# Performance work log

Measured on AMD Instinct MI355X. Metric: run time of the kernel, lower is better.

The kernel has to match this reference:

```python
import jax, jax.numpy as jnp
import numpy as np

LN_EPS = 1e-5
NUM_HEADS = 16

def _layernorm(x, g, b):
    mu = jnp.mean(x, axis=-1, keepdims=True)
    var = jnp.mean(jnp.square(x - mu), axis=-1, keepdims=True)
    return (x - mu) * jax.lax.rsqrt(var + LN_EPS) * g + b

def setup_inputs() -> dict:
    key = jax.random.key(0)
    ks = jax.random.split(key, 8)
    B, N, C, Hf = 8, 4096, 1024, 2048
    s = 1.0 / np.sqrt(C)
    return {
        "x": jax.random.normal(ks[0], (B, N, C), jnp.float32),
        "ln1_g": jnp.ones((C,), jnp.float32),
        "ln1_b": jnp.zeros((C,), jnp.float32),
        "ln2_g": jnp.ones((C,), jnp.float32),
        "ln2_b": jnp.zeros((C,), jnp.float32),
        "wq": jax.random.normal(ks[1], (C, C), jnp.float32) * s,
        "wk": jax.random.normal(ks[2], (C, C), jnp.float32) * s,
        "wv": jax.random.normal(ks[3], (C, C), jnp.float32) * s,
        "proj_w": jax.random.normal(ks[4], (C, C), jnp.float32) * s,
        "proj_b": jnp.zeros((C,), jnp.float32),
        "fc1_w": jax.random.normal(ks[5], (C, Hf), jnp.float32) * s,
        "fc1_b": jnp.zeros((Hf,), jnp.float32),
        "fc2_w": jax.random.normal(ks[6], (Hf, C), jnp.float32) / np.sqrt(Hf),
        "fc2_b": jnp.zeros((C,), jnp.float32),
    }

def reference(x, ln1_g, ln1_b, ln2_g, ln2_b, wq, wk, wv, proj_w, proj_b,
              fc1_w, fc1_b, fc2_w, fc2_b):
    B, N, C = x.shape
    H = NUM_HEADS
    d = C // H
    scale = d ** -0.5

    # --- attention branch (note: attention over the head_dim axis, d x d scores) ---
    h = _layernorm(x, ln1_g, ln1_b)
    def split(t):  # (B,N,C) -> (B,H,d,N), matching permute(0,2,3,1)
        return jnp.transpose(t.reshape(B, N, H, d), (0, 2, 3, 1))
    q = split(h @ wq)
    k = split(h @ wk)
    v = split(h @ wv)
    attn = jax.nn.softmax(jnp.einsum("bhdn,bhen->bhde", q, k) * scale, axis=-1)  # (B,H,d,d)
    o = jnp.einsum("bhde,bhen->bhdn", attn, v)           # (B,H,d,N)
    o = jnp.transpose(o, (0, 2, 1, 3)).reshape(B, N, C)  # transpose(1,2).reshape
    x = x + (o @ proj_w + proj_b)

    # --- MLP branch ---
    h2 = _layernorm(x, ln2_g, ln2_b)
    h2 = jax.nn.gelu(h2 @ fc1_w + fc1_b, approximate=False)
    x = x + (h2 @ fc2_w + fc2_b)
    return x
```

## Files before the change

### kernel.cpp

```cpp
#include <hip/hip_runtime.h>
#include <cmath>

typedef __attribute__((ext_vector_type(8))) _Float16 f16x8;
typedef __attribute__((ext_vector_type(8))) unsigned short u16x8;
typedef __attribute__((ext_vector_type(4))) float f32x4;

__device__ __forceinline__ unsigned short f2h(float f) {
  return __builtin_bit_cast(unsigned short, (_Float16)f);
}
__device__ __forceinline__ float h2f(unsigned short u) {
  return (float)__builtin_bit_cast(_Float16, u);
}

__device__ __forceinline__ void async16(const void* gp, void* lp) {
  __builtin_amdgcn_global_load_lds(
      (const __attribute__((address_space(1))) void*)gp,
      (__attribute__((address_space(3))) void*)lp, 16, 0, 0);
}

__global__ __launch_bounds__(256) void transpose_cast(
    const float* __restrict__ W, unsigned short* __restrict__ WT, int K, int N) {
  __shared__ float tile[32][33];
  const int tx = threadIdx.x & 31, ty = threadIdx.x >> 5;
  const int n0 = blockIdx.x * 32, k0 = blockIdx.y * 32;
#pragma unroll
  for (int r = 0; r < 4; ++r)
    tile[ty + 8 * r][tx] = W[(size_t)(k0 + ty + 8 * r) * N + n0 + tx];
  __syncthreads();
#pragma unroll
  for (int r = 0; r < 4; ++r)
    WT[(size_t)(n0 + ty + 8 * r) * K + k0 + tx] = f2h(tile[tx][ty + 8 * r]);
}

__global__ __launch_bounds__(256) void layernorm_cast(
    const float* __restrict__ x, const float* __restrict__ g,
    const float* __restrict__ bt, unsigned short* __restrict__ out) {
  const int row = blockIdx.x, tid = threadIdx.x;
  const float4 v = ((const float4*)(x + (size_t)row * 1024))[tid];
  float s = v.x + v.y + v.z + v.w;
  float ss = v.x * v.x + v.y * v.y + v.z * v.z + v.w * v.w;
#pragma unroll
  for (int off = 32; off >= 1; off >>= 1) {
    s += __shfl_down(s, off);
    ss += __shfl_down(ss, off);
  }
  __shared__ float red[10];
  const int wave = tid >> 6, lane = tid & 63;
  if (lane == 0) { red[wave] = s; red[4 + wave] = ss; }
  __syncthreads();
  if (tid == 0) {
    float S = red[0] + red[1] + red[2] + red[3];
    float SS = red[4] + red[5] + red[6] + red[7];
    float mu = S * (1.f / 1024.f);
    float var = SS * (1.f / 1024.f) - mu * mu;
    red[8] = mu;
    red[9] = rsqrtf(var + 1e-5f);
  }
  __syncthreads();
  const float mu = red[8], rs = red[9];
  const float4 gv = ((const float4*)g)[tid];
  const float4 bv = ((const float4*)bt)[tid];
  ushort4 r;
  r.x = f2h((v.x - mu) * rs * gv.x + bv.x);
  r.y = f2h((v.y - mu) * rs * gv.y + bv.y);
  r.z = f2h((v.z - mu) * rs * gv.z + bv.z);
  r.w = f2h((v.w - mu) * rs * gv.w + bv.w);
  ((ushort4*)(out + (size_t)row * 1024))[tid] = r;
}

__global__ __launch_bounds__(256) void resid_ln(
    const float* __restrict__ x, const unsigned short* __restrict__ pr,
    const float* __restrict__ pb, const float* __restrict__ g,
    const float* __restrict__ bt, float* __restrict__ out,
    unsigned short* __restrict__ h2) {
  const int row = blockIdx.x, tid = threadIdx.x;
  const size_t off = (size_t)row * 1024;
  const float4 xv = ((const float4*)(x + off))[tid];
  const ushort4 pv = ((const ushort4*)(pr + off))[tid];
  const float4 bb = ((const float4*)pb)[tid];
  float4 v;
  v.x = xv.x + h2f(pv.x) + bb.x;
  v.y = xv.y + h2f(pv.y) + bb.y;
  v.z = xv.z + h2f(pv.z) + bb.z;
  v.w = xv.w + h2f(pv.w) + bb.w;
  ((float4*)(out + off))[tid] = v;
  float s = v.x + v.y + v.z + v.w;
  float ss = v.x * v.x + v.y * v.y + v.z * v.z + v.w * v.w;
#pragma unroll
  for (int o = 32; o >= 1; o >>= 1) {
    s += __shfl_down(s, o);
    ss += __shfl_down(ss, o);
  }
  __shared__ float red[10];
  const int wave = tid >> 6, lane = tid & 63;
  if (lane == 0) { red[wave] = s; red[4 + wave] = ss; }
  __syncthreads();
  if (tid == 0) {
    float S = red[0] + red[1] + red[2] + red[3];
    float SS = red[4] + red[5] + red[6] + red[7];
    float mu = S * (1.f / 1024.f);
    float var = SS * (1.f / 1024.f) - mu * mu;
    red[8] = mu;
    red[9] = rsqrtf(var + 1e-5f);
  }
  __syncthreads();
  const float mu = red[8], rs = red[9];
  const float4 gv = ((const float4*)g)[tid];
  const float4 bv = ((const float4*)bt)[tid];
  ushort4 r;
  r.x = f2h((v.x - mu) * rs * gv.x + bv.x);
  r.y = f2h((v.y - mu) * rs * gv.y + bv.y);
  r.z = f2h((v.z - mu) * rs * gv.z + bv.z);
  r.w = f2h((v.w - mu) * rs * gv.w + bv.w);
  ((ushort4*)(h2 + off))[tid] = r;
}

__global__ __launch_bounds__(256) void resid_add(
    float* __restrict__ out, const unsigned short* __restrict__ y,
    const float* __restrict__ b) {
  const int row = blockIdx.x, tid = threadIdx.x;
  const size_t off = (size_t)row * 1024;
  float4 o = ((const float4*)(out + off))[tid];
  const ushort4 yv = ((const ushort4*)(y + off))[tid];
  const float4 bv = ((const float4*)b)[tid];
  o.x += h2f(yv.x) + bv.x;
  o.y += h2f(yv.y) + bv.y;
  o.z += h2f(yv.z) + bv.z;
  o.w += h2f(yv.w) + bv.w;
  ((float4*)(out + off))[tid] = o;
}

__global__ __launch_bounds__(256) void gemm_bt(
    const unsigned short* __restrict__ A, const unsigned short* __restrict__ BT,
    int M, int N, int K,
    const float* __restrict__ bias, unsigned short* __restrict__ outB, int gelu) {
  __shared__ unsigned short smem[17408];
  unsigned short* sA = smem;
  unsigned short* sB = smem + 8192;
  const int tid = threadIdx.x, wave = tid >> 6, lane = tid & 63;
  const int l16 = lane & 15, g16 = lane >> 4;
  const int wm = wave & 1, wn = wave >> 1;

  const int lin = blockIdx.y * gridDim.x + blockIdx.x;
  const int t_ = lin >> 3;
  const int bx = t_ % gridDim.x;
  const int by = (lin & 7) + 8 * (t_ / gridDim.x);
  const int row0 = by * 128, col0 = bx * 128;

  const int r_ = tid >> 2;
  const int s_ = ((tid & 3) ^ ((tid >> 3) & 3)) * 8;
  const unsigned short* pA = A + (size_t)(row0 + r_) * K + s_;
  const unsigned short* pB = BT + (size_t)(col0 + r_) * K + s_;
  unsigned short* dA = sA + wave * 512;
  unsigned short* dB = sB + wave * 512;
  const size_t rstep = (size_t)64 * K;

  f32x4 acc[4][4] = {};

  for (int k0 = 0; k0 < K; k0 += 64) {
    __syncthreads();
    async16(pA, dA);
    async16(pA + rstep, dA + 2048);
    async16(pA + 32, dA + 4096);
    async16(pA + rstep + 32, dA + 6144);
    async16(pB, dB);
    async16(pB + rstep, dB + 2048);
    async16(pB + 32, dB + 4096);
    async16(pB + rstep + 32, dB + 6144);
    pA += 64;
    pB += 64;
    __syncthreads();
#pragma unroll
    for (int kk = 0; kk < 2; ++kk) {
      f16x8 af[4], bf[4];
#pragma unroll
      for (int i = 0; i < 4; ++i) {
        const int ra = wm * 64 + i * 16 + l16;
        af[i] = __builtin_bit_cast(f16x8,
            *(const u16x8*)&sA[kk * 4096 + ra * 32 + (g16 ^ ((ra >> 1) & 3)) * 8]);
      }
#pragma unroll
      for (int j = 0; j < 4; ++j) {
        const int rb = wn * 64 + j * 16 + l16;
        bf[j] = __builtin_bit_cast(f16x8,
            *(const u16x8*)&sB[kk * 4096 + rb * 32 + (g16 ^ ((rb >> 1) & 3)) * 8]);
      }
#pragma unroll
      for (int i = 0; i < 4; ++i)
#pragma unroll
        for (int j = 0; j < 4; ++j)
          acc[i][j] = __builtin_amdgcn_mfma_f32_16x16x32_f16(af[i], bf[j], acc[i][j], 0, 0, 0);
    }
  }

  __syncthreads();
  unsigned short* scr = smem + wave * 4352;
#pragma unroll
  for (int j = 0; j < 4; ++j) {
    const float bcol = gelu ? bias[col0 + wn * 64 + j * 16 + l16] : 0.f;
#pragma unroll
    for (int i = 0; i < 4; ++i)
#pragma unroll
      for (int r = 0; r < 4; ++r) {
        float val = acc[i][j][r] + bcol;
        if (gelu) val = 0.5f * val * (1.0f + erff(val * 0.70710678118f));
        scr[(i * 16 + g16 * 4 + r) * 68 + j * 16 + l16] = f2h(val);
      }
  }
#pragma unroll
  for (int rr = 0; rr < 8; ++rr) {
    const int lr = rr * 8 + (lane >> 3);
    const int lc = (lane & 7) * 8;
    const u16x8 val = *(const u16x8*)&scr[lr * 68 + lc];
    *(u16x8*)(outB + (size_t)(row0 + wm * 64 + lr) * N + col0 + wn * 64 + lc) = val;
  }
}


#define STAGE_A(TT, KKH)                                                       \
  {                                                                            \
    unsigned short* d = smem + ((TT) & 1) * 32768 + (KKH) * 8192 + wave * 512; \
    const unsigned short* sp_ = pA + (size_t)(TT) * 64 + (KKH) * 32;           \
    async16(sp_, d);                                                           \
    async16(sp_ + rstep, d + 4096);                                            \
  }

#define STAGE_B(TT, KKH)                                                       \
  {                                                                            \
    unsigned short* d =                                                        \
        smem + ((TT) & 1) * 32768 + 16384 + (KKH) * 8192 + wave * 512;         \
    const unsigned short* sp_ = pB + (size_t)(TT) * 64 + (KKH) * 32;           \
    async16(sp_, d);                                                           \
    async16(sp_ + rstep, d + 4096);                                            \
  }

#define GPHASE(KK, MH, STAGE, TAILW)                                           \
  {                                                                            \
    f16x8 af[4];                                                               \
    _Pragma("unroll") for (int i = 0; i < 4; ++i) {                            \
      const int ra = wm * 128 + ((MH)*4 + i) * 16 + l16;                       \
      af[i] = __builtin_bit_cast(                                              \
          f16x8, *(const u16x8*)&bufA[(KK)*8192 + ra * 32 +                    \
                                      ((g16 ^ ((ra >> 1) & 3)) * 8)]);         \
    }                                                                          \
    if ((MH) == 0) {                                                           \
      _Pragma("unroll") for (int j = 0; j < 4; ++j) {                          \
        const int rb = wn * 64 + j * 16 + l16;                                 \
        bf[j] = __builtin_bit_cast(                                            \
            f16x8, *(const u16x8*)&bufB[(KK)*8192 + rb * 32 +                  \
                                        ((g16 ^ ((rb >> 1) & 3)) * 8)]);       \
      }                                                                        \
    }                                                                          \
    STAGE;                                                                     \
    __builtin_amdgcn_s_barrier();                                              \
    asm volatile("s_waitcnt lgkmcnt(0)" ::: "memory");                         \
    __builtin_amdgcn_s_setprio(1);                                             \
    _Pragma("unroll") for (int i = 0; i < 4; ++i)                              \
        _Pragma("unroll") for (int j = 0; j < 4; ++j) acc[(MH)*4 + i][j] =     \
        __builtin_amdgcn_mfma_f32_16x16x32_f16(af[i], bf[j],                   \
                                               acc[(MH)*4 + i][j], 0, 0, 0);   \
    __builtin_amdgcn_s_setprio(0);                                             \
    TAILW;                                                                     \
    __builtin_amdgcn_s_barrier();                                              \
  }

__global__ __launch_bounds__(512) void gemm256(
    const unsigned short* __restrict__ A, const unsigned short* __restrict__ BT,
    int M, int N, int K,
    const float* __restrict__ bias, unsigned short* __restrict__ outB, int gelu) {
  __shared__ __align__(16) unsigned short smem[65536];
  const int tid = threadIdx.x, wave = tid >> 6, lane = tid & 63;
  const int l16 = lane & 15, g16 = lane >> 4;
  const int wm = wave >> 2, wn = wave & 3;

  const int lin = blockIdx.y * gridDim.x + blockIdx.x;
  const int t_ = lin >> 3;
  const int bx = t_ % gridDim.x;
  const int by = (lin & 7) + 8 * (t_ / gridDim.x);
  const int row0 = by * 256, col0 = bx * 256;

  const int r_ = tid >> 2;
  const int s_ = ((tid & 3) ^ ((tid >> 3) & 3)) * 8;
  const unsigned short* pA = A + (size_t)(row0 + r_) * K + s_;
  const unsigned short* pB = BT + (size_t)(col0 + r_) * K + s_;
  const size_t rstep = (size_t)128 * K;
  const int NT = K >> 6;

  f32x4 acc[8][4] = {};

  STAGE_B(0, 0);
  STAGE_A(0, 0);
  STAGE_B(0, 1);
  STAGE_A(0, 1);
  STAGE_B(1, 0);
  STAGE_A(1, 0);
  STAGE_B(1, 1);
  asm volatile("s_waitcnt vmcnt(6)" ::: "memory");
  __builtin_amdgcn_s_barrier();

  for (int t = 0; t < NT - 2; ++t) {
    const unsigned short* bufA = smem + (t & 1) * 32768;
    const unsigned short* bufB = bufA + 16384;
    f16x8 bf[4];
    GPHASE(0, 0, STAGE_A(t + 1, 1), )
    GPHASE(0, 1, STAGE_B(t + 2, 0), )
    GPHASE(1, 0, STAGE_A(t + 2, 0), )
    GPHASE(1, 1, STAGE_B(t + 2, 1),
           asm volatile("s_waitcnt vmcnt(6)" ::: "memory"))
  }

  {
    const int t = NT - 2;
    const unsigned short* bufA = smem + (t & 1) * 32768;
    const unsigned short* bufB = bufA + 16384;
    f16x8 bf[4];
    GPHASE(0, 0, STAGE_A(t + 1, 1), )
    GPHASE(0, 1, , )
    GPHASE(1, 0, , )
    GPHASE(1, 1, , asm volatile("s_waitcnt vmcnt(0)" ::: "memory"))
  }
  {
    const int t = NT - 1;
    const unsigned short* bufA = smem + (t & 1) * 32768;
    const unsigned short* bufB = bufA + 16384;
    f16x8 bf[4];
    GPHASE(0, 0, , )
    GPHASE(0, 1, , )
    GPHASE(1, 0, , )
    GPHASE(1, 1, , )
  }

  unsigned short* scr = smem + wave * 4352;
#pragma unroll
  for (int mh = 0; mh < 2; ++mh) {
#pragma unroll
    for (int j = 0; j < 4; ++j) {
      const float bcol = gelu ? bias[col0 + wn * 64 + j * 16 + l16] : 0.f;
#pragma unroll
      for (int i = 0; i < 4; ++i)
#pragma unroll
        for (int r = 0; r < 4; ++r) {
          float val = acc[mh * 4 + i][j][r] + bcol;
          if (gelu) val = 0.5f * val * (1.0f + erff(val * 0.70710678118f));
          scr[(i * 16 + g16 * 4 + r) * 68 + j * 16 + l16] = f2h(val);
        }
    }
#pragma unroll
    for (int rr = 0; rr < 8; ++rr) {
      const int lr = rr * 8 + (lane >> 3);
      const int lc = (lane & 7) * 8;
      const u16x8 val = *(const u16x8*)&scr[lr * 68 + lc];
      *(u16x8*)(outB + (size_t)(row0 + wm * 128 + mh * 64 + lr) * N + col0 +
                wn * 64 + lc) = val;
    }
  }
}

__global__ __launch_bounds__(256) void attn_qk_part(
    const unsigned short* __restrict__ qkv, float* __restrict__ sp) {
  constexpr int ST = 72;
  __shared__ unsigned short sQT[64 * ST];
  __shared__ unsigned short sKT[64 * ST];
  const int bx = blockIdx.x, bh = bx >> 2, chunk = bx & 3;
  const int b = bh >> 4, h = bh & 15;
  const size_t base = (size_t)b * 4096 * 3072 + (size_t)h * 64;
  const int tid = threadIdx.x, wave = tid >> 6, lane = tid & 63;
  const int l16 = lane & 15, g16 = lane >> 4;
  const int wm = wave & 1, wn = wave >> 1;
  const int srow = tid >> 2, sseg = tid & 3;

  f32x4 acc[2][2] = {};

  for (int ntl = 0; ntl < 16; ++ntl) {
    const int nt = chunk * 16 + ntl;
    __syncthreads();
    const size_t roff = base + (size_t)(nt * 64 + srow) * 3072 + sseg * 16;
    const u16x8 q0 = *(const u16x8*)(qkv + roff);
    const u16x8 q1 = *(const u16x8*)(qkv + roff + 8);
    const u16x8 k0 = *(const u16x8*)(qkv + roff + 1024);
    const u16x8 k1 = *(const u16x8*)(qkv + roff + 1032);
#pragma unroll
    for (int ii = 0; ii < 8; ++ii) {
      sQT[(sseg * 16 + ii) * ST + srow] = q0[ii];
      sQT[(sseg * 16 + 8 + ii) * ST + srow] = q1[ii];
      sKT[(sseg * 16 + ii) * ST + srow] = k0[ii];
      sKT[(sseg * 16 + 8 + ii) * ST + srow] = k1[ii];
    }
    __syncthreads();
#pragma unroll
    for (int kk = 0; kk < 2; ++kk) {
      f16x8 aq[2], bk[2];
#pragma unroll
      for (int i = 0; i < 2; ++i)
        aq[i] = __builtin_bit_cast(f16x8,
            *(const u16x8*)&sQT[(wm * 32 + i * 16 + l16) * ST + kk * 32 + g16 * 8]);
#pragma unroll
      for (int j = 0; j < 2; ++j)
        bk[j] = __builtin_bit_cast(f16x8,
            *(const u16x8*)&sKT[(wn * 32 + j * 16 + l16) * ST + kk * 32 + g16 * 8]);
#pragma unroll
      for (int i = 0; i < 2; ++i)
#pragma unroll
        for (int j = 0; j < 2; ++j)
          acc[i][j] = __builtin_amdgcn_mfma_f32_16x16x32_f16(aq[i], bk[j], acc[i][j], 0, 0, 0);
    }
  }

  float* o = sp + (size_t)bx * 4096;
#pragma unroll
  for (int i = 0; i < 2; ++i)
#pragma unroll
    for (int j = 0; j < 2; ++j)
#pragma unroll
      for (int r = 0; r < 4; ++r)
        o[(wm * 32 + i * 16 + g16 * 4 + r) * 64 + (wn * 32 + j * 16 + l16)] = acc[i][j][r];
}

__global__ __launch_bounds__(64) void attn_softmax(
    const float* __restrict__ sp, unsigned short* __restrict__ am) {
  const int bh = blockIdx.x, dd = threadIdx.x;
  const float* p = sp + (size_t)bh * 4 * 4096 + dd * 64;
  float row[64];
#pragma unroll
  for (int e4 = 0; e4 < 16; ++e4) {
    const float4 a = ((const float4*)p)[e4];
    const float4 b_ = ((const float4*)(p + 4096))[e4];
    const float4 c_ = ((const float4*)(p + 8192))[e4];
    const float4 d_ = ((const float4*)(p + 12288))[e4];
    row[4 * e4 + 0] = a.x + b_.x + c_.x + d_.x;
    row[4 * e4 + 1] = a.y + b_.y + c_.y + d_.y;
    row[4 * e4 + 2] = a.z + b_.z + c_.z + d_.z;
    row[4 * e4 + 3] = a.w + b_.w + c_.w + d_.w;
  }
  float mx = -1e30f;
#pragma unroll
  for (int e = 0; e < 64; ++e) mx = fmaxf(mx, row[e]);
  float sum = 0.f;
#pragma unroll
  for (int e = 0; e < 64; ++e) {
    row[e] = __expf(0.125f * (row[e] - mx));
    sum += row[e];
  }
  const float inv = 1.0f / sum;
  unsigned short* q = am + (size_t)bh * 4096 + dd * 64;
#pragma unroll
  for (int e = 0; e < 64; ++e) q[e] = f2h(row[e] * inv);
}

__global__ __launch_bounds__(256) void attn_pv(
    const unsigned short* __restrict__ qkv, const unsigned short* __restrict__ am,
    unsigned short* __restrict__ o) {
  const int bx = blockIdx.x, bh = bx >> 2, chunk = bx & 3;
  const int b = bh >> 4, h = bh & 15;
  const size_t base = (size_t)b * 4096 * 3072 + (size_t)h * 64;
  const int tid = threadIdx.x, wave = tid >> 6, lane = tid & 63;
  const int l16 = lane & 15, g16 = lane >> 4;
  const int wm = wave & 1, wn = wave >> 1;

  f16x8 amf[2][2];
#pragma unroll
  for (int i = 0; i < 2; ++i)
#pragma unroll
    for (int kk = 0; kk < 2; ++kk)
      amf[i][kk] = __builtin_bit_cast(f16x8,
          *(const u16x8*)(am + (size_t)bh * 4096 +
                          (wm * 32 + i * 16 + l16) * 64 + kk * 32 + g16 * 8));

  for (int ntl = 0; ntl < 16; ++ntl) {
    const int nt = chunk * 16 + ntl;
    f32x4 oc[2][2] = {};
#pragma unroll
    for (int kk = 0; kk < 2; ++kk) {
#pragma unroll
      for (int j = 0; j < 2; ++j) {
        const f16x8 vf = __builtin_bit_cast(f16x8,
            *(const u16x8*)(qkv + base + 2048 +
                            (size_t)(nt * 64 + wn * 32 + j * 16 + l16) * 3072 +
                            kk * 32 + g16 * 8));
#pragma unroll
        for (int i = 0; i < 2; ++i)
          oc[i][j] = __builtin_amdgcn_mfma_f32_16x16x32_f16(amf[i][kk], vf, oc[i][j], 0, 0, 0);
      }
    }
#pragma unroll
    for (int i = 0; i < 2; ++i)
#pragma unroll
      for (int j = 0; j < 2; ++j)
#pragma unroll
        for (int r = 0; r < 4; ++r) {
          const int dd = wm * 32 + i * 16 + g16 * 4 + r;
          const int nf = nt * 64 + wn * 32 + j * 16 + l16;
          const int row = b * 4096 + dd * 64 + h * 4 + (nf >> 10);
          o[(size_t)row * 1024 + (nf & 1023)] = f2h(oc[i][j][r]);
        }
  }
}

extern "C" void kernel_launch(void* const* d_in, const int* in_sizes, int n_in,
                              void* d_out, int out_size, void* d_ws, size_t ws_size,
                              hipStream_t stream) {
  (void)in_sizes; (void)n_in; (void)out_size; (void)ws_size;
  const float* x = (const float*)d_in[0];
  const float* ln1g = (const float*)d_in[1];
  const float* ln1b = (const float*)d_in[2];
  const float* ln2g = (const float*)d_in[3];
  const float* ln2b = (const float*)d_in[4];
  const float* wq = (const float*)d_in[5];
  const float* wk = (const float*)d_in[6];
  const float* wv = (const float*)d_in[7];
  const float* projw = (const float*)d_in[8];
  const float* projb = (const float*)d_in[9];
  const float* fc1w = (const float*)d_in[10];
  const float* fc1b = (const float*)d_in[11];
  const float* fc2w = (const float*)d_in[12];
  const float* fc2b = (const float*)d_in[13];
  float* out = (float*)d_out;

  const int M = 8 * 4096, C = 1024, HF = 2048;
  const size_t MC = (size_t)M * C;

  unsigned short* p = (unsigned short*)d_ws;
  unsigned short* wqkvT = p; p += (size_t)3 * C * C;
  unsigned short* prT = p; p += (size_t)C * C;
  unsigned short* f1T = p; p += (size_t)HF * C;
  unsigned short* f2T = p; p += (size_t)C * HF;
  unsigned short* hb = p;  p += MC;
  unsigned short* qkvb = p; p += 3 * MC;
  float* Spart = (float*)hb;
  unsigned short* Am = wqkvT;
  unsigned short* ob = hb;
  unsigned short* projout = qkvb;
  unsigned short* h2 = qkvb + 2 * MC;
  unsigned short* h3 = qkvb;
  unsigned short* yb = hb;

  transpose_cast<<<dim3(C / 32, C / 32), 256, 0, stream>>>(wq, wqkvT, C, C);
  transpose_cast<<<dim3(C / 32, C / 32), 256, 0, stream>>>(wk, wqkvT + (size_t)C * C, C, C);
  transpose_cast<<<dim3(C / 32, C / 32), 256, 0, stream>>>(wv, wqkvT + (size_t)2 * C * C, C, C);
  transpose_cast<<<dim3(C / 32, C / 32), 256, 0, stream>>>(projw, prT, C, C);
  transpose_cast<<<dim3(HF / 32, C / 32), 256, 0, stream>>>(fc1w, f1T, C, HF);
  transpose_cast<<<dim3(C / 32, HF / 32), 256, 0, stream>>>(fc2w, f2T, HF, C);

  layernorm_cast<<<M, 256, 0, stream>>>(x, ln1g, ln1b, hb);

  gemm256<<<dim3(3 * C / 256, M / 256), 512, 0, stream>>>(
      hb, wqkvT, M, 3 * C, C, nullptr, qkvb, 0);

  attn_qk_part<<<512, 256, 0, stream>>>(qkvb, Spart);
  attn_softmax<<<128, 64, 0, stream>>>(Spart, Am);
  attn_pv<<<512, 256, 0, stream>>>(qkvb, Am, ob);

  gemm_bt<<<dim3(C / 128, M / 128), 256, 0, stream>>>(
      ob, prT, M, C, C, nullptr, projout, 0);

  resid_ln<<<M, 256, 0, stream>>>(x, projout, projb, ln2g, ln2b, out, h2);

  gemm256<<<dim3(HF / 256, M / 256), 512, 0, stream>>>(
      h2, f1T, M, HF, C, fc1b, h3, 1);

  gemm256<<<dim3(C / 256, M / 256), 512, 0, stream>>>(
      h3, f2T, M, C, HF, nullptr, yb, 0);

  resid_add<<<M, 256, 0, stream>>>(out, yb, fc2b);
}
```

Measured before the change: 1.135 ms.

## Batch weight transposes, parallelize softmax per wave, use 256-tile GEMM for proj

Merges the six weight transpose-cast launches into one 3D-grid launch that takes a struct of per-matrix arguments and exits early on out-of-range tiles. Rewrites the attention softmax so each wave handles one row, with one element per lane and shuffle reductions, replacing 128 single-wave blocks that each looped serially over 64 elements. Routes the output projection through the existing 256x256 GEMM kernel and deletes the 128-tile gemm_bt. The batched transpose launches many empty blocks for the smaller matrices, and the larger projection tile gives fewer blocks on the N=1024 problem.

```diff
diff --git a/kernel.cpp b/kernel.cpp
--- a/kernel.cpp
+++ b/kernel.cpp
@@ -18,11 +18,22 @@
       (__attribute__((address_space(3))) void*)lp, 16, 0, 0);
 }
 
-__global__ __launch_bounds__(256) void transpose_cast(
-    const float* __restrict__ W, unsigned short* __restrict__ WT, int K, int N) {
+struct TCArgs {
+  const float* W[6];
+  unsigned short* T[6];
+  int K[6];
+  int N[6];
+};
+
+__global__ __launch_bounds__(256) void transpose_cast6(TCArgs a) {
+  const int z = blockIdx.z;
+  const int K = a.K[z], N = a.N[z];
+  const int n0 = blockIdx.x * 32, k0 = blockIdx.y * 32;
+  if (n0 >= N || k0 >= K) return;
+  const float* __restrict__ W = a.W[z];
+  unsigned short* __restrict__ WT = a.T[z];
   __shared__ float tile[32][33];
   const int tx = threadIdx.x & 31, ty = threadIdx.x >> 5;
-  const int n0 = blockIdx.x * 32, k0 = blockIdx.y * 32;
 #pragma unroll
   for (int r = 0; r < 4; ++r)
     tile[ty + 8 * r][tx] = W[(size_t)(k0 + ty + 8 * r) * N + n0 + tx];
@@ -128,92 +139,6 @@
   o.z += h2f(yv.z) + bv.z;
   o.w += h2f(yv.w) + bv.w;
   ((float4*)(out + off))[tid] = o;
-}
-
-__global__ __launch_bounds__(256) void gemm_bt(
-    const unsigned short* __restrict__ A, const unsigned short* __restrict__ BT,
-    int M, int N, int K,
-    const float* __restrict__ bias, unsigned short* __restrict__ outB, int gelu) {
-  __shared__ unsigned short smem[17408];
-  unsigned short* sA = smem;
-  unsigned short* sB = smem + 8192;
-  const int tid = threadIdx.x, wave = tid >> 6, lane = tid & 63;
-  const int l16 = lane & 15, g16 = lane >> 4;
-  const int wm = wave & 1, wn = wave >> 1;
-
-  const int lin = blockIdx.y * gridDim.x + blockIdx.x;
-  const int t_ = lin >> 3;
-  const int bx = t_ % gridDim.x;
-  const int by = (lin & 7) + 8 * (t_ / gridDim.x);
-  const int row0 = by * 128, col0 = bx * 128;
-
-  const int r_ = tid >> 2;
-  const int s_ = ((tid & 3) ^ ((tid >> 3) & 3)) * 8;
-  const unsigned short* pA = A + (size_t)(row0 + r_) * K + s_;
-  const unsigned short* pB = BT + (size_t)(col0 + r_) * K + s_;
-  unsigned short* dA = sA + wave * 512;
-  unsigned short* dB = sB + wave * 512;
-  const size_t rstep = (size_t)64 * K;
-
-  f32x4 acc[4][4] = {};
-
-  for (int k0 = 0; k0 < K; k0 += 64) {
-    __syncthreads();
-    async16(pA, dA);
-    async16(pA + rstep, dA + 2048);
-    async16(pA + 32, dA + 4096);
-    async16(pA + rstep + 32, dA + 6144);
-    async16(pB, dB);
-    async16(pB + rstep, dB + 2048);
-    async16(pB + 32, dB + 4096);
-    async16(pB + rstep + 32, dB + 6144);
-    pA += 64;
-    pB += 64;
-    __syncthreads();
-#pragma unroll
-    for (int kk = 0; kk < 2; ++kk) {
-      f16x8 af[4], bf[4];
-#pragma unroll
-      for (int i = 0; i < 4; ++i) {
-        const int ra = wm * 64 + i * 16 + l16;
-        af[i] = __builtin_bit_cast(f16x8,
-            *(const u16x8*)&sA[kk * 4096 + ra * 32 + (g16 ^ ((ra >> 1) & 3)) * 8]);
-      }
-#pragma unroll
-      for (int j = 0; j < 4; ++j) {
-        const int rb = wn * 64 + j * 16 + l16;
-        bf[j] = __builtin_bit_cast(f16x8,
-            *(const u16x8*)&sB[kk * 4096 + rb * 32 + (g16 ^ ((rb >> 1) & 3)) * 8]);
-      }
-#pragma unroll
-      for (int i = 0; i < 4; ++i)
-#pragma unroll
-        for (int j = 0; j < 4; ++j)
-          acc[i][j] = __builtin_amdgcn_mfma_f32_16x16x32_f16(af[i], bf[j], acc[i][j], 0, 0, 0);
-    }
-  }
-
-  __syncthreads();
-  unsigned short* scr = smem + wave * 4352;
-#pragma unroll
-  for (int j = 0; j < 4; ++j) {
-    const float bcol = gelu ? bias[col0 + wn * 64 + j * 16 + l16] : 0.f;
-#pragma unroll
-    for (int i = 0; i < 4; ++i)
-#pragma unroll
-      for (int r = 0; r < 4; ++r) {
-        float val = acc[i][j][r] + bcol;
-        if (gelu) val = 0.5f * val * (1.0f + erff(val * 0.70710678118f));
-        scr[(i * 16 + g16 * 4 + r) * 68 + j * 16 + l16] = f2h(val);
-      }
-  }
-#pragma unroll
-  for (int rr = 0; rr < 8; ++rr) {
-    const int lr = rr * 8 + (lane >> 3);
-    const int lc = (lane & 7) * 8;
-    const u16x8 val = *(const u16x8*)&scr[lr * 68 + lc];
-    *(u16x8*)(outB + (size_t)(row0 + wm * 64 + lr) * N + col0 + wn * 64 + lc) = val;
-  }
 }
 
 
@@ -416,35 +341,21 @@
         o[(wm * 32 + i * 16 + g16 * 4 + r) * 64 + (wn * 32 + j * 16 + l16)] = acc[i][j][r];
 }
 
-__global__ __launch_bounds__(64) void attn_softmax(
+__global__ __launch_bounds__(256) void attn_softmax(
     const float* __restrict__ sp, unsigned short* __restrict__ am) {
-  const int bh = blockIdx.x, dd = threadIdx.x;
-  const float* p = sp + (size_t)bh * 4 * 4096 + dd * 64;
-  float row[64];
-#pragma unroll
-  for (int e4 = 0; e4 < 16; ++e4) {
-    const float4 a = ((const float4*)p)[e4];
-    const float4 b_ = ((const float4*)(p + 4096))[e4];
-    const float4 c_ = ((const float4*)(p + 8192))[e4];
-    const float4 d_ = ((const float4*)(p + 12288))[e4];
-    row[4 * e4 + 0] = a.x + b_.x + c_.x + d_.x;
-    row[4 * e4 + 1] = a.y + b_.y + c_.y + d_.y;
-    row[4 * e4 + 2] = a.z + b_.z + c_.z + d_.z;
-    row[4 * e4 + 3] = a.w + b_.w + c_.w + d_.w;
-  }
-  float mx = -1e30f;
-#pragma unroll
-  for (int e = 0; e < 64; ++e) mx = fmaxf(mx, row[e]);
-  float sum = 0.f;
-#pragma unroll
-  for (int e = 0; e < 64; ++e) {
-    row[e] = __expf(0.125f * (row[e] - mx));
-    sum += row[e];
-  }
-  const float inv = 1.0f / sum;
-  unsigned short* q = am + (size_t)bh * 4096 + dd * 64;
-#pragma unroll
-  for (int e = 0; e < 64; ++e) q[e] = f2h(row[e] * inv);
+  const int gid = blockIdx.x * 4 + (threadIdx.x >> 6);
+  const int lane = threadIdx.x & 63;
+  const int bh = gid >> 6, dd = gid & 63;
+  const float* p = sp + (size_t)bh * 16384 + dd * 64 + lane;
+  const float v = p[0] + p[4096] + p[8192] + p[12288];
+  float mx = v;
+#pragma unroll
+  for (int o = 32; o >= 1; o >>= 1) mx = fmaxf(mx, __shfl_xor(mx, o));
+  const float e = __expf(0.125f * (v - mx));
+  float s = e;
+#pragma unroll
+  for (int o = 32; o >= 1; o >>= 1) s += __shfl_xor(s, o);
+  am[(size_t)bh * 4096 + dd * 64 + lane] = f2h(e / s);
 }
 
 __global__ __launch_bounds__(256) void attn_pv(
@@ -534,12 +445,14 @@
   unsigned short* h3 = qkvb;
   unsigned short* yb = hb;
 
-  transpose_cast<<<dim3(C / 32, C / 32), 256, 0, stream>>>(wq, wqkvT, C, C);
-  transpose_cast<<<dim3(C / 32, C / 32), 256, 0, stream>>>(wk, wqkvT + (size_t)C * C, C, C);
-  transpose_cast<<<dim3(C / 32, C / 32), 256, 0, stream>>>(wv, wqkvT + (size_t)2 * C * C, C, C);
-  transpose_cast<<<dim3(C / 32, C / 32), 256, 0, stream>>>(projw, prT, C, C);
-  transpose_cast<<<dim3(HF / 32, C / 32), 256, 0, stream>>>(fc1w, f1T, C, HF);
-  transpose_cast<<<dim3(C / 32, HF / 32), 256, 0, stream>>>(fc2w, f2T, HF, C);
+  TCArgs ta;
+  ta.W[0] = wq;    ta.T[0] = wqkvT;                     ta.K[0] = C;  ta.N[0] = C;
+  ta.W[1] = wk;    ta.T[1] = wqkvT + (size_t)C * C;     ta.K[1] = C;  ta.N[1] = C;
+  ta.W[2] = wv;    ta.T[2] = wqkvT + (size_t)2 * C * C; ta.K[2] = C;  ta.N[2] = C;
+  ta.W[3] = projw; ta.T[3] = prT;                       ta.K[3] = C;  ta.N[3] = C;
+  ta.W[4] = fc1w;  ta.T[4] = f1T;                       ta.K[4] = C;  ta.N[4] = HF;
+  ta.W[5] = fc2w;  ta.T[5] = f2T;                       ta.K[5] = HF; ta.N[5] = C;
+  transpose_cast6<<<dim3(HF / 32, HF / 32, 6), 256, 0, stream>>>(ta);
 
   layernorm_cast<<<M, 256, 0, stream>>>(x, ln1g, ln1b, hb);
 
@@ -547,10 +460,10 @@
       hb, wqkvT, M, 3 * C, C, nullptr, qkvb, 0);
 
   attn_qk_part<<<512, 256, 0, stream>>>(qkvb, Spart);
-  attn_softmax<<<128, 64, 0, stream>>>(Spart, Am);
+  attn_softmax<<<2048, 256, 0, stream>>>(Spart, Am);
   attn_pv<<<512, 256, 0, stream>>>(qkvb, Am, ob);
 
-  gemm_bt<<<dim3(C / 128, M / 128), 256, 0, stream>>>(
+  gemm256<<<dim3(C / 256, M / 256), 512, 0, stream>>>(
       ob, prT, M, C, C, nullptr, projout, 0);
 
   resid_ln<<<M, 256, 0, stream>>>(x, projout, projb, ln2g, ln2b, out, h2);
```

After: 1.145 ms. Within noise of the previous version (+0.9%).
